# Kernel tuning notes

Measured on AMD Instinct MI355X. Metric: run time of the kernel, lower is better.

The kernel has to match this reference:

```python
import jax, jax.numpy as jnp
import numpy as np

H = 2048      # hidden_dim
NH = 32       # num_heads
HD = H // NH  # head_dim


def setup_inputs() -> dict:
    key = jax.random.key(0)
    ks = jax.random.split(key, 9)
    s = 1.0 / np.sqrt(H)
    return {
        "hidden_states": jax.random.normal(ks[0], (2, 2048, H), dtype=jnp.float32),
        "wq": jax.random.uniform(ks[1], (H, H), jnp.float32, -s, s),
        "bq": jnp.zeros((H,), jnp.float32),
        "wk": jax.random.uniform(ks[2], (H, H), jnp.float32, -s, s),
        "bk": jnp.zeros((H,), jnp.float32),
        "wv": jax.random.uniform(ks[3], (H, H), jnp.float32, -s, s),
        "bv": jnp.zeros((H,), jnp.float32),
        "wo": jax.random.uniform(ks[4], (H, H), jnp.float32, -s, s),
        "bo": jnp.zeros((H,), jnp.float32),
    }


def reference(hidden_states, wq, bq, wk, bk, wv, bv, wo, bo):
    B, S, _ = hidden_states.shape
    def heads(x):  # [B,S,H] -> [B,NH,S,HD]
        return x.reshape(B, S, NH, HD).transpose(0, 2, 1, 3)
    q = heads(hidden_states @ wq.T + bq)
    k = heads(hidden_states @ wk.T + bk)
    v = heads(hidden_states @ wv.T + bv)
    scores = jnp.einsum("bhqd,bhkd->bhqk", q, k) / np.sqrt(HD).astype(np.float32)
    causal = jnp.tril(jnp.ones((S, S), dtype=bool))
    scores = jnp.where(causal, scores, -jnp.inf)
    attn = jax.nn.softmax(scores, axis=-1)
    out = jnp.einsum("bhqk,bhkd->bhqd", attn, v)
    out = out.transpose(0, 2, 1, 3).reshape(B, S, H)
    return out @ wo.T + bo
```

## Files before the change

### kernel.cpp

```cpp
#include <hip/hip_runtime.h>
#include <hip/hip_bf16.h>

#define HDIM 2048
#define NHEADS 32
#define HEADD 64
#define NBATCH 2
#define SEQLEN 2048
#define MTOT (NBATCH * SEQLEN)
#define NQT (SEQLEN / 128)
#define LDQKV 6144

typedef __bf16 bf16;
typedef __bf16 bf16x8 __attribute__((ext_vector_type(8)));
typedef float f32x4 __attribute__((ext_vector_type(4)));
typedef float f32x8 __attribute__((ext_vector_type(8)));
typedef float f32x16 __attribute__((ext_vector_type(16)));

__device__ __forceinline__ void gload_lds16(const bf16* g, bf16* l) {
  __builtin_amdgcn_global_load_lds(
      (const __attribute__((address_space(1))) void*)g,
      (__attribute__((address_space(3))) void*)l, 16, 0, 0);
}

__device__ __forceinline__ unsigned cvtpk_bf16(float lo, float hi) {
  unsigned r;
  asm("v_cvt_pk_bf16_f32 %0, %1, %2" : "=v"(r) : "v"(lo), "v"(hi));
  return r;
}

__device__ __forceinline__ float max3f(float a, float b, float c) {
  float r;
  asm("v_max3_f32 %0, %1, %2, %3" : "=v"(r) : "v"(a), "v"(b), "v"(c));
  return r;
}

__global__ void __launch_bounds__(256) cvt_f32_to_bf16(
    const float* __restrict__ src, bf16* __restrict__ dst, int n) {
  int i = (blockIdx.x * 256 + threadIdx.x) * 8;
  if (i >= n) return;
  f32x8 a = *(const f32x8*)(src + i);
  bf16x8 o;
#pragma unroll
  for (int j = 0; j < 8; ++j) o[j] = (bf16)a[j];
  *(bf16x8*)(dst + i) = o;
}

__global__ void __launch_bounds__(256) cvt4_f32_to_bf16(
    const float* __restrict__ s0, const float* __restrict__ s1,
    const float* __restrict__ s2, const float* __restrict__ s3,
    bf16* __restrict__ d0, bf16* __restrict__ d1,
    bf16* __restrict__ d2, bf16* __restrict__ d3) {
  const float* src; bf16* dst;
  switch (blockIdx.y) {
    case 0: src = s0; dst = d0; break;
    case 1: src = s1; dst = d1; break;
    case 2: src = s2; dst = d2; break;
    default: src = s3; dst = d3; break;
  }
  int i = (blockIdx.x * 256 + threadIdx.x) * 8;
  f32x8 a = *(const f32x8*)(src + i);
  bf16x8 o;
#pragma unroll
  for (int j = 0; j < 8; ++j) o[j] = (bf16)a[j];
  *(bf16x8*)(dst + i) = o;
}

__global__ void __launch_bounds__(256) pack_bias(
    const float* __restrict__ bq, const float* __restrict__ bk,
    const float* __restrict__ bv, float* __restrict__ out) {
  int i = blockIdx.x * 256 + threadIdx.x;
  if (i >= LDQKV) return;
  float v;
  if (i < HDIM) v = bq[i];
  else if (i < 2 * HDIM) v = bk[i - HDIM];
  else v = bv[i - 2 * HDIM];
  out[i] = v;
}

template <int BM, bool OUT_F32>
__global__ void __launch_bounds__(512, 2) gemm3(
    const bf16* __restrict__ A, const bf16* __restrict__ W,
    const float* __restrict__ bias, void* __restrict__ Cout,
    int Ndim, float scale) {
  constexpr int NT = 64;
  constexpr int FM = BM / 32;
  constexpr int ALD = BM / 128;
  constexpr int LPT = ALD + 2;
  constexpr int MPX = (4096 / BM) / 8;
  __shared__ bf16 As[4][BM * 32];
  __shared__ bf16 Bs[4][256 * 32];

  const int tid = threadIdx.x;
  const int l = tid & 63;
  const int w = tid >> 6;
  const int wm = w >> 2;
  const int wn = w & 3;

  const int wid = blockIdx.x;
  const int j = wid >> 3;
  const int m0 = ((wid & 7) * MPX + (j & (MPX - 1))) * BM;
  const int n0 = (j / MPX) * 256;

  const float secsc = (n0 < 2048) ? scale : 1.0f;

  const int rowA = tid >> 2;
  const int cg = (((tid & 3) ^ ((tid >> 3) & 3))) * 8;

  auto stageA = [&](int s, int kt) {
    const int k0 = kt * 32 + cg;
#pragma unroll
    for (int i = 0; i < ALD; ++i)
      gload_lds16(A + (size_t)(m0 + i * 128 + rowA) * 2048 + k0,
                  &As[s][(i * 512 + w * 64) * 8]);
  };
  auto stageB = [&](int s, int kt) {
    const int k0 = kt * 32 + cg;
#pragma unroll
    for (int i = 0; i < 2; ++i)
      gload_lds16(W + (size_t)(n0 + i * 128 + rowA) * 2048 + k0,
                  &Bs[s][(i * 512 + w * 64) * 8]);
  };

  f32x4 acc[FM][4];
#pragma unroll
  for (int mf = 0; mf < FM; ++mf)
#pragma unroll
    for (int nf = 0; nf < 4; ++nf) acc[mf][nf] = {0.f, 0.f, 0.f, 0.f};

  const int fr = l & 15;
  const int fch = (((l >> 4) ^ ((fr >> 1) & 3))) * 8;

  stageA(0, 0); stageB(0, 0);
  stageA(1, 1); stageB(1, 1);
  stageA(2, 2); stageB(2, 2);
  if constexpr (LPT == 4)
    asm volatile("s_waitcnt vmcnt(8)" ::: "memory");
  else
    asm volatile("s_waitcnt vmcnt(6)" ::: "memory");
  __builtin_amdgcn_s_barrier();

  for (int t = 0; t < NT; ++t) {
    const int s = t & 3;
    const int sn = (t + 3) & 3;
    const bool st = (t + 3) < NT;

    bf16x8 bf[4], af[FM];
#pragma unroll
    for (int nf = 0; nf < 4; ++nf)
      bf[nf] = *(const bf16x8*)&Bs[s][(wn * 64 + nf * 16 + fr) * 32 + fch];
#pragma unroll
    for (int f = 0; f < FM; ++f)
      af[f] = *(const bf16x8*)&As[s][(wm * (BM / 2) + f * 16 + fr) * 32 + fch];

    if (st) { stageA(sn, t + 3); stageB(sn, t + 3); }

    __builtin_amdgcn_s_setprio(1);
#pragma unroll
    for (int f = 0; f < FM; ++f)
#pragma unroll
      for (int nf = 0; nf < 4; ++nf)
        acc[f][nf] = __builtin_amdgcn_mfma_f32_16x16x32_bf16(
            af[f], bf[nf], acc[f][nf], 0, 0, 0);
    __builtin_amdgcn_s_setprio(0);

    if (t < NT - 3) {
      if constexpr (LPT == 4)
        asm volatile("s_waitcnt vmcnt(8)" ::: "memory");
      else
        asm volatile("s_waitcnt vmcnt(6)" ::: "memory");
    } else if (t == NT - 3) {
      if constexpr (LPT == 4)
        asm volatile("s_waitcnt vmcnt(4)" ::: "memory");
      else
        asm volatile("s_waitcnt vmcnt(3)" ::: "memory");
    } else if (t == NT - 2) {
      asm volatile("s_waitcnt vmcnt(0)" ::: "memory");
    }
    if (t < NT - 1) __builtin_amdgcn_s_barrier();
  }

  const int rj = (l >> 4) * 4;
#pragma unroll
  for (int mf = 0; mf < FM; ++mf)
#pragma unroll
    for (int nf = 0; nf < 4; ++nf) {
      const int col = n0 + wn * 64 + nf * 16 + fr;
      const float bvl = bias[col];
#pragma unroll
      for (int jj = 0; jj < 4; ++jj) {
        const int row = m0 + wm * (BM / 2) + mf * 16 + rj + jj;
        const float v = (acc[mf][nf][jj] + bvl) * secsc;
        if constexpr (OUT_F32)
          ((float*)Cout)[(size_t)row * Ndim + col] = v;
        else
          ((bf16*)Cout)[(size_t)row * Ndim + col] = (bf16)v;
      }
    }
}

__global__ void __launch_bounds__(256) transpose_v(
    const bf16* __restrict__ QKV, bf16* __restrict__ Vt) {
  __shared__ bf16 T[64][72];
  const int t = threadIdx.x;
  const int s0 = blockIdx.x * 64;
  const int h = blockIdx.y, b = blockIdx.z;
  const size_t inb = (size_t)b * SEQLEN * LDQKV + 2 * HDIM + (size_t)h * HEADD;
#pragma unroll
  for (int i = 0; i < 2; ++i) {
    const int idx = t + i * 256;
    const int r = idx >> 3, c = (idx & 7) * 8;
    *(bf16x8*)&T[r][c] = *(const bf16x8*)&QKV[inb + (size_t)(s0 + r) * LDQKV + c];
  }
  __syncthreads();
  const size_t outb = (size_t)(b * NHEADS + h) * HEADD * SEQLEN + s0;
#pragma unroll
  for (int i = 0; i < 2; ++i) {
    const int idx = t + i * 256;
    const int d = idx >> 3, cs = (idx & 7) * 8;
    bf16x8 o;
#pragma unroll
    for (int j = 0; j < 8; ++j) o[j] = T[cs + j][d];
    *(bf16x8*)&Vt[outb + (size_t)d * SEQLEN + cs] = o;
  }
}

__global__ void __launch_bounds__(256) attn4(
    const bf16* __restrict__ QKV, const bf16* __restrict__ Vt,
    bf16* __restrict__ O) {
  __shared__ bf16 Kl[2][64 * 64];
  __shared__ bf16 Vl[2][64 * 64];

  const int tid = threadIdx.x;
  const int l = tid & 63;
  const int w = tid >> 6;
  const int lq = l & 31;
  const int g = l >> 5;
  const int h = blockIdx.y, b = blockIdx.z;
  const size_t baseQ = (size_t)b * SEQLEN * LDQKV + (size_t)h * HEADD;
  const size_t baseK = baseQ + HDIM;
  const size_t baseV = (size_t)(b * NHEADS + h) * HEADD * SEQLEN;
  const size_t baseO = (size_t)b * SEQLEN * HDIM + (size_t)h * HEADD;

  const int L0 = w * 128 + l;
  const int L1 = w * 128 + 64 + l;
  const int r0 = L0 >> 3, gc0 = ((L0 & 7) ^ (r0 & 7)) * 8;
  const int r1 = L1 >> 3, gc1 = ((L1 & 7) ^ (r1 & 7)) * 8;
  const int dst0 = (w * 128) * 8;
  const int dst1 = (w * 128 + 64) * 8;

  auto stage = [&](int bufi, int kt) {
    const int k0s = kt * 64;
    gload_lds16(QKV + baseK + (size_t)(k0s + r0) * LDQKV + gc0, &Kl[bufi][dst0]);
    gload_lds16(QKV + baseK + (size_t)(k0s + r1) * LDQKV + gc1, &Kl[bufi][dst1]);
    gload_lds16(Vt + baseV + (size_t)r0 * SEQLEN + k0s + gc0, &Vl[bufi][dst0]);
    gload_lds16(Vt + baseV + (size_t)r1 * SEQLEN + k0s + gc1, &Vl[bufi][dst1]);
  };

#pragma unroll
  for (int seg = 0; seg < 2; ++seg) {
    const int qt = seg ? blockIdx.x : (NQT - 1 - blockIdx.x);
    const int q0 = qt * 128;
    const int qw = q0 + w * 32;
    const int qa = qw + lq;

    bf16x8 qf[4];
#pragma unroll
    for (int ks = 0; ks < 4; ++ks)
      qf[ks] = *(const bf16x8*)&QKV[baseQ + (size_t)qa * LDQKV + ks * 16 + g * 8];

    f32x16 oacc0, oacc1;
#pragma unroll
    for (int r = 0; r < 16; ++r) { oacc0[r] = 0.f; oacc1[r] = 0.f; }
    float mrun = -__builtin_inff(), lrun = 0.f;

    const int nkt = q0 / 64 + 2;
    stage(0, 0);

    for (int kt = 0; kt < nkt; ++kt) {
      const int cur = kt & 1;
      const int k0 = kt * 64;
      if (kt + 1 < nkt) {
        stage(cur ^ 1, kt + 1);
        asm volatile("s_waitcnt vmcnt(4)" ::: "memory");
      } else {
        asm volatile("s_waitcnt vmcnt(0)" ::: "memory");
      }
      __builtin_amdgcn_s_barrier();

      if (k0 <= qw + 31) {
        f32x16 st0, st1;
#pragma unroll
        for (int r = 0; r < 16; ++r) { st0[r] = 0.f; st1[r] = 0.f; }
        __builtin_amdgcn_s_setprio(1);
#pragma unroll
        for (int ks = 0; ks < 4; ++ks) {
          const int cr = (((2 * ks + g) ^ (lq & 7))) * 8;
          bf16x8 kf0 = *(const bf16x8*)&Kl[cur][lq * 64 + cr];
          bf16x8 kf1 = *(const bf16x8*)&Kl[cur][(32 + lq) * 64 + cr];
          st0 = __builtin_amdgcn_mfma_f32_32x32x16_bf16(kf0, qf[ks], st0, 0, 0, 0);
          st1 = __builtin_amdgcn_mfma_f32_32x32x16_bf16(kf1, qf[ks], st1, 0, 0, 0);
        }
        __builtin_amdgcn_s_setprio(0);

        if (k0 + 63 > qw) {
#pragma unroll
          for (int r = 0; r < 16; ++r) {
            const int ro = (r & 3) + 8 * (r >> 2) + 4 * g;
            if (k0 + ro > qa) st0[r] = -__builtin_inff();
            if (k0 + 32 + ro > qa) st1[r] = -__builtin_inff();
          }
        }

        float mx[8];
#pragma unroll
        for (int r = 0; r < 8; ++r)
          mx[r] = fmaxf(max3f(st0[r], st0[r + 8], st1[r]), st1[r + 8]);
        const float ma = max3f(mx[0], mx[1], mx[2]);
        const float mb = max3f(mx[3], mx[4], mx[5]);
        const float mc = max3f(mx[6], mx[7], ma);
        const float mtree = fmaxf(mb, mc);
        const float pm = fmaxf(mtree, __shfl_xor(mtree, 32));

        const float mnew = fmaxf(mrun, pm);
        if (!__all(pm - mrun <= 11.0f)) {
          const float sc = __builtin_amdgcn_exp2f(mrun - mnew);
          lrun *= sc;
#pragma unroll
          for (int r = 0; r < 16; ++r) {
            const int ro = (r & 3) + 8 * (r >> 2) + 4 * g;
            const float scr = __shfl(sc, ro);
            oacc0[r] *= scr;
            oacc1[r] *= scr;
          }
          mrun = mnew;
        }

#pragma unroll
        for (int r = 0; r < 16; ++r) {
          st0[r] = __builtin_amdgcn_exp2f(st0[r] - mrun);
          st1[r] = __builtin_amdgcn_exp2f(st1[r] - mrun);
        }
        float sm[8];
#pragma unroll
        for (int r = 0; r < 8; ++r)
          sm[r] = (st0[r] + st0[r + 8]) + (st1[r] + st1[r + 8]);
#pragma unroll
        for (int s = 4; s > 0; s >>= 1)
#pragma unroll
          for (int r = 0; r < 4; ++r)
            if (r < s) sm[r] += sm[r + s];
        lrun += sm[0] + __shfl_xor(sm[0], 32);

        unsigned wd0[8], wd1[8];
#pragma unroll
        for (int i = 0; i < 8; ++i) {
          wd0[i] = cvtpk_bf16(st0[2 * i], st0[2 * i + 1]);
          wd1[i] = cvtpk_bf16(st1[2 * i], st1[2 * i + 1]);
        }
        bf16x8 paf[4];
#pragma unroll
        for (int kt2 = 0; kt2 < 2; ++kt2)
#pragma unroll
          for (int hf = 0; hf < 2; ++hf) {
            const unsigned* wsrc = kt2 ? wd1 : wd0;
            const unsigned a0 = wsrc[hf * 4 + 0], a1 = wsrc[hf * 4 + 1];
            const unsigned b0 = wsrc[hf * 4 + 2], b1 = wsrc[hf * 4 + 3];
            const unsigned sb0 = (unsigned)__shfl_xor((int)b0, 32);
            const unsigned sb1 = (unsigned)__shfl_xor((int)b1, 32);
            const unsigned sa0 = (unsigned)__shfl_xor((int)a0, 32);
            const unsigned sa1 = (unsigned)__shfl_xor((int)a1, 32);
            union { unsigned u[4]; bf16x8 v; } fu;
            fu.u[0] = g ? sb0 : a0;
            fu.u[1] = g ? sb1 : a1;
            fu.u[2] = g ? b0 : sa0;
            fu.u[3] = g ? b1 : sa1;
            paf[kt2 * 2 + hf] = fu.v;
          }

        __builtin_amdgcn_s_setprio(1);
#pragma unroll
        for (int s = 0; s < 4; ++s) {
          const int cr = (((2 * s + g) ^ (lq & 7))) * 8;
          bf16x8 vf0 = *(const bf16x8*)&Vl[cur][lq * 64 + cr];
          bf16x8 vf1 = *(const bf16x8*)&Vl[cur][(32 + lq) * 64 + cr];
          oacc0 = __builtin_amdgcn_mfma_f32_32x32x16_bf16(paf[s], vf0, oacc0, 0, 0, 0);
          oacc1 = __builtin_amdgcn_mfma_f32_32x32x16_bf16(paf[s], vf1, oacc1, 0, 0, 0);
        }
        __builtin_amdgcn_s_setprio(0);
      }
      __builtin_amdgcn_s_barrier();
    }

#pragma unroll
    for (int r = 0; r < 16; ++r) {
      const int ro = (r & 3) + 8 * (r >> 2) + 4 * g;
      const float lr = __shfl(lrun, ro);
      const float inv = 1.0f / lr;
      O[baseO + (size_t)(qw + ro) * HDIM + lq] = (bf16)(oacc0[r] * inv);
      O[baseO + (size_t)(qw + ro) * HDIM + 32 + lq] = (bf16)(oacc1[r] * inv);
    }
  }
}

extern "C" void kernel_launch(void* const* d_in, const int* in_sizes, int n_in,
                              void* d_out, int out_size, void* d_ws, size_t ws_size,
                              hipStream_t stream) {
  (void)in_sizes; (void)n_in; (void)out_size; (void)ws_size;
  const float* hs = (const float*)d_in[0];
  const float* wq = (const float*)d_in[1];
  const float* bq = (const float*)d_in[2];
  const float* wk = (const float*)d_in[3];
  const float* bk = (const float*)d_in[4];
  const float* wv = (const float*)d_in[5];
  const float* bv = (const float*)d_in[6];
  const float* wo = (const float*)d_in[7];
  const float* bo = (const float*)d_in[8];

  char* wsp = (char*)d_ws;
  bf16* hsb  = (bf16*)wsp; wsp += (size_t)MTOT * HDIM * sizeof(bf16);
  bf16* wqb  = (bf16*)wsp; wsp += (size_t)HDIM * HDIM * sizeof(bf16);
  bf16* wkb  = (bf16*)wsp; wsp += (size_t)HDIM * HDIM * sizeof(bf16);
  bf16* wvb  = (bf16*)wsp; wsp += (size_t)HDIM * HDIM * sizeof(bf16);
  bf16* wob  = (bf16*)wsp; wsp += (size_t)HDIM * HDIM * sizeof(bf16);
  bf16* QKVb = (bf16*)wsp; wsp += (size_t)MTOT * LDQKV * sizeof(bf16);
  float* biasqkv = (float*)wsp; wsp += (size_t)LDQKV * sizeof(float);
  bf16* aob = hsb;
  bf16* Vtb = wqb;

  const int nHS = MTOT * HDIM;
  const int nW = HDIM * HDIM;
  cvt_f32_to_bf16<<<nHS / 2048, 256, 0, stream>>>(hs, hsb, nHS);
  dim3 gc(nW / 2048, 4);
  cvt4_f32_to_bf16<<<gc, 256, 0, stream>>>(wq, wk, wv, wo, wqb, wkb, wvb, wob);
  pack_bias<<<LDQKV / 256, 256, 0, stream>>>(bq, bk, bv, biasqkv);

  gemm3<256, false><<<dim3(16 * (LDQKV / 256)), 512, 0, stream>>>(
      hsb, wqb, biasqkv, QKVb, LDQKV, 0.125f * 1.44269504f);

  dim3 gt(SEQLEN / 64, NHEADS, NBATCH);
  transpose_v<<<gt, 256, 0, stream>>>(QKVb, Vtb);

  dim3 ga(NQT / 2, NHEADS, NBATCH);
  attn4<<<ga, 256, 0, stream>>>(QKVb, Vtb, aob);

  gemm3<128, true><<<dim3(32 * (HDIM / 256)), 512, 0, stream>>>(
      aob, wob, bo, (float*)d_out, HDIM, 1.0f);
}
```

Baseline: 262.7 us.

## Add ping-pong 256x256 QKV GEMM with quadrant-interleaved loads and MFMA

Adds a new QKV projection GEMM kernel that computes a 256x256 tile as four 128x128 quadrants. K-step staging is 64 wide and uses XOR-swizzled LDS, with the async global-to-LDS loads for the next steps interleaved between quadrant MFMA phases. Barriers and setprio are used to schedule the phases. The aim is to overlap memory traffic with MFMA work and cut the number of K iterations compared with the previous 32-wide staging. In exchange it uses more barriers per iteration and depends on a fragile vmcnt-based wait scheme. Only the QKV GEMM is switched over; the output projection still uses the old kernel.

```diff
diff --git a/kernel.cpp b/kernel.cpp
--- a/kernel.cpp
+++ b/kernel.cpp
@@ -75,6 +75,144 @@
   else if (i < 2 * HDIM) v = bk[i - HDIM];
   else v = bv[i - 2 * HDIM];
   out[i] = v;
+}
+
+template <bool OUT_F32>
+__global__ void __launch_bounds__(512, 2) gemm8p(
+    const bf16* __restrict__ A, const bf16* __restrict__ W,
+    const float* __restrict__ bias, void* __restrict__ Cout,
+    int Ndim, float scale) {
+  constexpr int NT = 32;
+  __shared__ bf16 As[2][2][128 * 64];
+  __shared__ bf16 Bs[2][2][128 * 64];
+
+  const int tid = threadIdx.x;
+  const int l = tid & 63;
+  const int w = tid >> 6;
+  const int wm = w >> 2;
+  const int wn = w & 3;
+
+  const int wid = blockIdx.x;
+  const int j = wid >> 3;
+  const int m0 = ((wid & 7) * 2 + (j & 1)) * 256;
+  const int n0 = (j >> 1) * 256;
+  const float secsc = (n0 < 2048) ? scale : 1.0f;
+
+  const int r_ = tid >> 3;
+  const int cs = (((tid & 7) ^ ((tid >> 3) & 7))) * 8;
+
+  auto stgA = [&](int slot, int half, int kt) {
+    const bf16* g = A + (size_t)(m0 + half * 128) * 2048 + kt * 64 + cs;
+#pragma unroll
+    for (int i = 0; i < 2; ++i)
+      gload_lds16(g + (size_t)(i * 64 + r_) * 2048,
+                  &As[slot][half][(i * 512 + w * 64) * 8]);
+  };
+  auto stgB = [&](int slot, int half, int kt) {
+    const bf16* g = W + (size_t)(n0 + half * 128) * 2048 + kt * 64 + cs;
+#pragma unroll
+    for (int i = 0; i < 2; ++i)
+      gload_lds16(g + (size_t)(i * 64 + r_) * 2048,
+                  &Bs[slot][half][(i * 512 + w * 64) * 8]);
+  };
+
+  f32x4 acc[2][2][4][2];
+#pragma unroll
+  for (int qm = 0; qm < 2; ++qm)
+#pragma unroll
+    for (int qn = 0; qn < 2; ++qn)
+#pragma unroll
+      for (int mf = 0; mf < 4; ++mf)
+#pragma unroll
+        for (int nf = 0; nf < 2; ++nf) acc[qm][qn][mf][nf] = {0.f, 0.f, 0.f, 0.f};
+
+  const int fr = l & 15;
+  const int ch0 = (((l >> 4)) ^ (fr & 7)) * 8;
+  const int ch1 = (((l >> 4) + 4) ^ (fr & 7)) * 8;
+
+#define RD_A(DST, SLOT, HALF)                                                  \
+  _Pragma("unroll") for (int mf = 0; mf < 4; ++mf) {                           \
+    const int rb = (wm * 64 + mf * 16 + fr) * 64;                              \
+    DST[mf][0] = *(const bf16x8*)&As[SLOT][HALF][rb + ch0];                    \
+    DST[mf][1] = *(const bf16x8*)&As[SLOT][HALF][rb + ch1];                    \
+  }
+#define RD_B(DST, SLOT, HALF)                                                  \
+  _Pragma("unroll") for (int nf = 0; nf < 2; ++nf) {                           \
+    const int rb = (wn * 32 + nf * 16 + fr) * 64;                              \
+    DST[nf][0] = *(const bf16x8*)&Bs[SLOT][HALF][rb + ch0];                    \
+    DST[nf][1] = *(const bf16x8*)&Bs[SLOT][HALF][rb + ch1];                    \
+  }
+#define MFMA_Q(QM, QN, AR, BR)                                                 \
+  __builtin_amdgcn_s_setprio(1);                                               \
+  _Pragma("unroll") for (int mf = 0; mf < 4; ++mf)                             \
+      _Pragma("unroll") for (int nf = 0; nf < 2; ++nf)                         \
+          _Pragma("unroll") for (int ks = 0; ks < 2; ++ks)                     \
+              acc[QM][QN][mf][nf] = __builtin_amdgcn_mfma_f32_16x16x32_bf16(   \
+                  AR[mf][ks], BR[nf][ks], acc[QM][QN][mf][nf], 0, 0, 0);       \
+  __builtin_amdgcn_s_setprio(0);
+
+  stgA(0, 0, 0); stgB(0, 0, 0); stgB(0, 1, 0); stgA(0, 1, 0);
+  stgA(1, 0, 1); stgB(1, 0, 1); stgB(1, 1, 1);
+  asm volatile("s_waitcnt vmcnt(6)" ::: "memory");
+  __builtin_amdgcn_s_barrier();
+
+  for (int t = 0; t < NT; ++t) {
+    const int s = t & 1;
+    bf16x8 a0[4][2], a1[4][2], b0[2][2], b1[2][2];
+
+    RD_A(a0, s, 0);
+    RD_B(b0, s, 0);
+    if (t + 1 < NT) stgA(s ^ 1, 1, t + 1);
+    __builtin_amdgcn_s_barrier();
+    MFMA_Q(0, 0, a0, b0);
+    __builtin_amdgcn_s_barrier();
+
+    RD_B(b1, s, 1);
+    if (t + 2 < NT) stgA(s, 0, t + 2);
+    __builtin_amdgcn_s_barrier();
+    MFMA_Q(0, 1, a0, b1);
+    __builtin_amdgcn_s_barrier();
+
+    RD_A(a1, s, 1);
+    if (t + 2 < NT) stgB(s, 0, t + 2);
+    __builtin_amdgcn_s_barrier();
+    MFMA_Q(1, 1, a1, b1);
+    __builtin_amdgcn_s_barrier();
+
+    if (t + 2 < NT) stgB(s, 1, t + 2);
+    __builtin_amdgcn_s_barrier();
+    MFMA_Q(1, 0, a1, b0);
+    if (t < NT - 2)
+      asm volatile("s_waitcnt vmcnt(6)" ::: "memory");
+    else
+      asm volatile("s_waitcnt vmcnt(0)" ::: "memory");
+    __builtin_amdgcn_s_barrier();
+  }
+#undef RD_A
+#undef RD_B
+#undef MFMA_Q
+
+  const int rj = (l >> 4) * 4;
+#pragma unroll
+  for (int qm = 0; qm < 2; ++qm)
+#pragma unroll
+    for (int qn = 0; qn < 2; ++qn)
+#pragma unroll
+      for (int mf = 0; mf < 4; ++mf)
+#pragma unroll
+        for (int nf = 0; nf < 2; ++nf) {
+          const int col = n0 + qn * 128 + wn * 32 + nf * 16 + fr;
+          const float bvl = bias[col];
+#pragma unroll
+          for (int jj = 0; jj < 4; ++jj) {
+            const int row = m0 + qm * 128 + wm * 64 + mf * 16 + rj + jj;
+            const float v = (acc[qm][qn][mf][nf][jj] + bvl) * secsc;
+            if constexpr (OUT_F32)
+              ((float*)Cout)[(size_t)row * Ndim + col] = v;
+            else
+              ((bf16*)Cout)[(size_t)row * Ndim + col] = (bf16)v;
+          }
+        }
 }
 
 template <int BM, bool OUT_F32>
@@ -434,7 +572,7 @@
   cvt4_f32_to_bf16<<<gc, 256, 0, stream>>>(wq, wk, wv, wo, wqb, wkb, wvb, wob);
   pack_bias<<<LDQKV / 256, 256, 0, stream>>>(bq, bk, bv, biasqkv);
 
-  gemm3<256, false><<<dim3(16 * (LDQKV / 256)), 512, 0, stream>>>(
+  gemm8p<false><<<dim3(16 * (LDQKV / 256)), 512, 0, stream>>>(
       hsb, wqb, biasqkv, QKVb, LDQKV, 0.125f * 1.44269504f);
 
   dim3 gt(SEQLEN / 64, NHEADS, NBATCH);
```

After: 260.8 us. Within noise of the previous version (-0.7%).

## Add dedicated QKV projection GEMM with 256x192 tiles and asymmetric buffering

Applied to the files above, without the earlier changes.

Replaces the QKV projection GEMM with a new 256-thread kernel. Each block computes a 256x192 output tile: 512 tiles in total, mapped in an interleaved order so neighbouring blocks share A rows. A is double-buffered and B is triple-buffered in LDS, with MFMA issue at raised priority. This aims to improve occupancy and wave balance over the previous 512-thread, 256x256 tile kernel. The epilogue writes bf16 with scalar stores, which may cost store bandwidth. The larger per-wave accumulator footprint (8x6 fragments) adds register pressure.

```diff
diff --git a/kernel.cpp b/kernel.cpp
--- a/kernel.cpp
+++ b/kernel.cpp
@@ -77,6 +77,128 @@
   out[i] = v;
 }
 
+template <bool OUT_F32>
+__global__ void __launch_bounds__(256, 2) gemmq(
+    const bf16* __restrict__ A, const bf16* __restrict__ W,
+    const float* __restrict__ bias, void* __restrict__ Cout,
+    int Ndim, float scale) {
+  constexpr int NT = 64;
+  __shared__ bf16 As[2][256 * 32];
+  __shared__ bf16 Bs[3][192 * 32];
+
+  const int tid = threadIdx.x;
+  const int l = tid & 63;
+  const int w = tid >> 6;
+  const int wm = w >> 1;
+  const int wn = w & 1;
+
+  const int wid = blockIdx.x;
+  const int j = wid >> 3;
+  const int m0 = ((wid & 7) * 2 + (j & 1)) * 256;
+  const int n0 = (j >> 1) * 192;
+
+  const int rowA = tid >> 2;
+  const int cg = (((tid & 3) ^ ((tid >> 3) & 3))) * 8;
+
+  auto stgA = [&](int s, int kt) {
+    const bf16* g = A + (size_t)m0 * 2048 + kt * 32 + cg;
+#pragma unroll
+    for (int i = 0; i < 4; ++i)
+      gload_lds16(g + (size_t)(i * 64 + rowA) * 2048,
+                  &As[s][(i * 256 + w * 64) * 8]);
+  };
+  auto stgB = [&](int s, int kt) {
+    const bf16* g = W + (size_t)n0 * 2048 + kt * 32 + cg;
+#pragma unroll
+    for (int i = 0; i < 3; ++i)
+      gload_lds16(g + (size_t)(i * 64 + rowA) * 2048,
+                  &Bs[s][(i * 256 + w * 64) * 8]);
+  };
+
+  f32x4 acc[8][6];
+#pragma unroll
+  for (int mf = 0; mf < 8; ++mf)
+#pragma unroll
+    for (int nf = 0; nf < 6; ++nf) acc[mf][nf] = {0.f, 0.f, 0.f, 0.f};
+
+  const int fr = l & 15;
+  const int fch = (((l >> 4) ^ ((fr >> 1) & 3))) * 8;
+  const int abase = (wm * 128 + fr) * 32 + fch;
+  const int bbase = (wn * 96 + fr) * 32 + fch;
+
+  stgA(0, 0);
+  stgB(0, 0);
+  stgB(1, 1);
+  asm volatile("s_waitcnt vmcnt(3)" ::: "memory");
+  __builtin_amdgcn_s_barrier();
+
+  int sb = 0;
+  for (int t = 0; t < NT; ++t) {
+    const int sa = t & 1;
+    int sb2 = sb + 2; if (sb2 >= 3) sb2 -= 3;
+
+    bf16x8 bf[6], af[4];
+#pragma unroll
+    for (int nf = 0; nf < 6; ++nf)
+      bf[nf] = *(const bf16x8*)&Bs[sb][bbase + nf * 16 * 32];
+#pragma unroll
+    for (int f = 0; f < 4; ++f)
+      af[f] = *(const bf16x8*)&As[sa][abase + f * 16 * 32];
+
+    if (t + 1 < NT) stgA(sa ^ 1, t + 1);
+    if (t + 2 < NT) stgB(sb2, t + 2);
+
+    __builtin_amdgcn_s_setprio(1);
+#pragma unroll
+    for (int f = 0; f < 4; ++f)
+#pragma unroll
+      for (int nf = 0; nf < 6; ++nf)
+        acc[f][nf] = __builtin_amdgcn_mfma_f32_16x16x32_bf16(
+            af[f], bf[nf], acc[f][nf], 0, 0, 0);
+    __builtin_amdgcn_s_setprio(0);
+
+#pragma unroll
+    for (int f = 0; f < 4; ++f)
+      af[f] = *(const bf16x8*)&As[sa][abase + (4 + f) * 16 * 32];
+
+    __builtin_amdgcn_s_setprio(1);
+#pragma unroll
+    for (int f = 0; f < 4; ++f)
+#pragma unroll
+      for (int nf = 0; nf < 6; ++nf)
+        acc[4 + f][nf] = __builtin_amdgcn_mfma_f32_16x16x32_bf16(
+            af[f], bf[nf], acc[4 + f][nf], 0, 0, 0);
+    __builtin_amdgcn_s_setprio(0);
+
+    if (t < NT - 2)
+      asm volatile("s_waitcnt vmcnt(3)" ::: "memory");
+    else
+      asm volatile("s_waitcnt vmcnt(0)" ::: "memory");
+    __builtin_amdgcn_s_barrier();
+
+    sb = (sb == 2) ? 0 : sb + 1;
+  }
+
+  const int rj = (l >> 4) * 4;
+#pragma unroll
+  for (int mf = 0; mf < 8; ++mf)
+#pragma unroll
+    for (int nf = 0; nf < 6; ++nf) {
+      const int col = n0 + wn * 96 + nf * 16 + fr;
+      const float secsc = (col < 2048) ? scale : 1.0f;
+      const float bvl = bias[col];
+#pragma unroll
+      for (int jj = 0; jj < 4; ++jj) {
+        const int row = m0 + wm * 128 + mf * 16 + rj + jj;
+        const float v = (acc[mf][nf][jj] + bvl) * secsc;
+        if constexpr (OUT_F32)
+          ((float*)Cout)[(size_t)row * Ndim + col] = v;
+        else
+          ((bf16*)Cout)[(size_t)row * Ndim + col] = (bf16)v;
+      }
+    }
+}
+
 template <int BM, bool OUT_F32>
 __global__ void __launch_bounds__(512, 2) gemm3(
     const bf16* __restrict__ A, const bf16* __restrict__ W,
@@ -434,7 +556,7 @@
   cvt4_f32_to_bf16<<<gc, 256, 0, stream>>>(wq, wk, wv, wo, wqb, wkb, wvb, wob);
   pack_bias<<<LDQKV / 256, 256, 0, stream>>>(bq, bk, bv, biasqkv);
 
-  gemm3<256, false><<<dim3(16 * (LDQKV / 256)), 512, 0, stream>>>(
+  gemmq<false><<<dim3(512), 256, 0, stream>>>(
       hsb, wqb, biasqkv, QKVb, LDQKV, 0.125f * 1.44269504f);
 
   dim3 gt(SEQLEN / 64, NHEADS, NBATCH);
```

Result: faster. 245.1 us (-6.7%).
